# Kernel tuning notes

Measured on AMD Instinct MI355X. Metric: run time of the kernel, lower is better.

The kernel has to match this reference:

```python
import jax, jax.numpy as jnp
import numpy as np

EPS = 1e-5  # torch BatchNorm2d default eps

def _bn(x, gamma, beta):
    # training-mode batch statistics over (N,H,W), per channel (biased variance)
    mean = jnp.mean(x, axis=(0, 2, 3), keepdims=True)
    var = jnp.var(x, axis=(0, 2, 3), keepdims=True)
    return gamma[None, :, None, None] * (x - mean) * jax.lax.rsqrt(var + EPS) + beta[None, :, None, None]

def _conv1x1(x, w, b):
    # (B,C,H,W) x (O,C) -> (B,O,H,W)
    return jnp.einsum('bchw,oc->bohw', x, w) + b[None, :, None, None]

def _maxpool2(x):
    B, C, H, W = x.shape
    return x.reshape(B, C, H // 2, 2, W // 2, 2).max(axis=(3, 5))

def setup_inputs() -> dict:
    key = jax.random.key(0)
    ks = jax.random.split(key, 5)
    B, C, H, W = 16, 256, 56, 56
    Ci, Cg = C // 8, C // 4
    def kaiming(k, o, i):
        return jax.random.normal(k, (o, i), jnp.float32) * np.float32(np.sqrt(2.0 / i))
    return {
        'x': jax.random.normal(ks[0], (B, C, H, W), jnp.float32),
        'bn1_gamma': jnp.ones((C,), jnp.float32),
        'bn1_beta': jnp.zeros((C,), jnp.float32),
        'w_g': kaiming(ks[1], Cg, C), 'b_g': jnp.zeros((Cg,), jnp.float32),
        'w_theta': kaiming(ks[2], Ci, C), 'b_theta': jnp.zeros((Ci,), jnp.float32),
        'w_phi': kaiming(ks[3], Ci, C), 'b_phi': jnp.zeros((Ci,), jnp.float32),
        'bn2_gamma': jnp.ones((Cg,), jnp.float32),
        'bn2_beta': jnp.zeros((Cg,), jnp.float32),
        'w_z': kaiming(ks[4], C, Cg), 'b_z': jnp.zeros((C,), jnp.float32),
    }

def reference(x, bn1_gamma, bn1_beta, w_g, b_g, w_theta, b_theta, w_phi, b_phi, bn2_gamma, bn2_beta, w_z, b_z):
    identity = x
    B, C, H, W = x.shape
    xa = jax.nn.relu(_bn(x, bn1_gamma, bn1_beta))
    g_x = _maxpool2(_conv1x1(xa, w_g, b_g))        # (B,Cg,H/2,W/2)
    phi_x = _maxpool2(_conv1x1(xa, w_phi, b_phi))  # (B,Ci,H/2,W/2)
    theta_x = _conv1x1(xa, w_theta, b_theta)       # (B,Ci,H,W)
    Cg = g_x.shape[1]
    Ci = theta_x.shape[1]
    Np = g_x.shape[2] * g_x.shape[3]               # subsampled positions (H/2*W/2)
    g_x = g_x.reshape(B, Cg, Np).transpose(0, 2, 1)      # (B,Np,Cg)
    phi_x = phi_x.reshape(B, Ci, Np)                     # (B,Ci,Np)
    theta_x = theta_x.reshape(B, Ci, H * W).transpose(0, 2, 1)  # (B,HW,Ci)
    f_div_C = jnp.einsum('bnc,bcm->bnm', theta_x, phi_x) / Np   # (B,HW,Np)
    y = jnp.einsum('bnm,bmc->bnc', f_div_C, g_x)                # (B,HW,Cg)
    y = y.transpose(0, 2, 1).reshape(B, Cg, H, W)
    w_y = _conv1x1(jax.nn.relu(_bn(y, bn2_gamma, bn2_beta)), w_z, b_z)
    return w_y + identity
```

## Files before the change

### kernel.cpp

```cpp
#include <hip/hip_runtime.h>
#include <hip/hip_bf16.h>

#define BB 16
#define CC 256
#define HWN 3136
#define NCI 32
#define NPP 784

typedef __attribute__((ext_vector_type(8))) short short8;
typedef __attribute__((ext_vector_type(4))) float floatx4;

__device__ __forceinline__ unsigned short f2bf(float f) {
    union { __hip_bfloat16 h; unsigned short u; } cv;
    cv.h = __float2bfloat16(f);
    return cv.u;
}
__device__ __forceinline__ float bf2f(unsigned short u) {
    return __uint_as_float(((unsigned)u) << 16);
}

__device__ __forceinline__ void stage_Tt(unsigned short* Tt, const unsigned short* th,
                                         int b, int hw0, int tid) {
    int p2 = tid & 15, hwq = tid >> 4;
    int c0 = 2 * p2;
    const unsigned short* tb = th + (size_t)(b * NCI) * HWN + hw0 + hwq * 4;
    ushort4 v0 = *(const ushort4*)(tb + (size_t)c0 * HWN);
    ushort4 v1 = *(const ushort4*)(tb + (size_t)(c0 + 1) * HWN);
    unsigned int* tw = (unsigned int*)Tt;
    tw[(hwq * 4 + 0) * 20 + p2] = (unsigned)v0.x | ((unsigned)v1.x << 16);
    tw[(hwq * 4 + 1) * 20 + p2] = (unsigned)v0.y | ((unsigned)v1.y << 16);
    tw[(hwq * 4 + 2) * 20 + p2] = (unsigned)v0.z | ((unsigned)v1.z << 16);
    tw[(hwq * 4 + 3) * 20 + p2] = (unsigned)v0.w | ((unsigned)v1.w << 16);
}

__global__ __launch_bounds__(256) void k_head(const float* __restrict__ x,
                                              const float* __restrict__ w_t,
                                              const float* __restrict__ w_p,
                                              const float* __restrict__ w_g,
                                              const float* __restrict__ w_z,
                                              unsigned short* __restrict__ wcat,
                                              unsigned short* __restrict__ wzb,
                                              unsigned short* __restrict__ pool,
                                              float* __restrict__ zacc,
                                              float* __restrict__ bn1part) {
    int blk = blockIdx.x;
    int c = threadIdx.x;
    if (blk < 128) {
        int o = blk;
        const float* src = (o < 32) ? (w_t + o * CC)
                          : (o < 64) ? (w_p + (o - 32) * CC)
                                     : (w_g + (o - 64) * CC);
        wcat[o * CC + c] = f2bf(src[c]);
        {
            int r = o * 2 + (c >> 7);
            int kk = c & 127;
            if (kk < 72)
                wzb[r * 72 + kk] = (kk < 64) ? f2bf(w_z[r * 64 + kk]) : (unsigned short)0;
        }
        if (o < 96) {
            int b = c >> 4, kk = c & 15;
            pool[((size_t)(b * 96 + o)) * 800 + 784 + kk] = 0;
        }
        int idx = o * 256 + c;
        if (idx < 17024) zacc[idx] = 0.f;
        return;
    }
    int bc = blk - 128;
    const float4* p = (const float4*)(x + (size_t)bc * HWN);
    int tid = c;
    float s = 0.f, q = 0.f;
    for (int i = tid; i < 784; i += 256) {
        float4 v = p[i];
        s += v.x + v.y + v.z + v.w;
        q += v.x * v.x + v.y * v.y + v.z * v.z + v.w * v.w;
    }
    #pragma unroll
    for (int off = 32; off > 0; off >>= 1) {
        s += __shfl_down(s, off);
        q += __shfl_down(q, off);
    }
    __shared__ float sh[16];
    int wid = tid >> 6, lane = tid & 63;
    if (lane == 0) { sh[wid] = s; sh[8 + wid] = q; }
    __syncthreads();
    if (tid == 0) bn1part[bc]        = sh[0] + sh[1] + sh[2] + sh[3];
    if (tid == 1) bn1part[4096 + bc] = sh[8] + sh[9] + sh[10] + sh[11];
}

__global__ __launch_bounds__(512) void k_conv1(const float* __restrict__ x,
                                               const unsigned short* __restrict__ wcat,
                                               const float* __restrict__ bn1part,
                                               const float* __restrict__ gamma,
                                               const float* __restrict__ beta,
                                               const float* __restrict__ b_g,
                                               const float* __restrict__ b_t,
                                               const float* __restrict__ b_p,
                                               unsigned short* __restrict__ th,
                                               unsigned short* __restrict__ pool,
                                               float* __restrict__ T1g,
                                               float* __restrict__ Gg) {
    int b  = blockIdx.y;
    int bx = blockIdx.x;
    int hw0 = bx * 112;
    int tid = threadIdx.x;
    int wv = tid >> 6, ln = tid & 63;
    int col = ln & 15, quad = ln >> 4;

    __shared__ unsigned short smem[128 * 120];
    unsigned short* As = smem;
    unsigned short* Bs = smem + 4096;
    __shared__ float ab_s[512];
    __shared__ float bias_s[128];

    if (tid < 256) {
        const float inv = 1.0f / (BB * HWN);
        float s = 0.f, q = 0.f;
        #pragma unroll
        for (int b2 = 0; b2 < BB; ++b2) {
            s += bn1part[b2 * 256 + tid];
            q += bn1part[4096 + b2 * 256 + tid];
        }
        float mean = s * inv;
        float var  = q * inv - mean * mean;
        float a = gamma[tid] * rsqrtf(var + 1e-5f);
        ab_s[tid] = a;
        ab_s[CC + tid] = beta[tid] - mean * a;
    }
    if (tid < 128) {
        int o = tid;
        bias_s[o] = (o < 32) ? b_t[o] : (o < 64) ? b_p[o - 32] : b_g[o - 64];
    }
    __syncthreads();

    floatx4 acc[7];
    #pragma unroll
    for (int nt = 0; nt < 7; ++nt)
        acc[nt] = (floatx4){0.f, 0.f, 0.f, 0.f};

    int p   = tid & 15;
    int hwq = tid >> 4;
    bool act = hwq < 28;
    const float* xb = x + (size_t)(b * CC) * HWN + hw0;

    float4 pv0, pv1;
    if (act) {
        int c0 = 2 * p;
        pv0 = *(const float4*)(xb + (size_t)c0 * HWN + hwq * 4);
        pv1 = *(const float4*)(xb + (size_t)(c0 + 1) * HWN + hwq * 4);
    }

    for (int k0 = 0; k0 < CC; k0 += 32) {
        {
            const unsigned short* gp = wcat + (wv * 16 + (ln >> 2)) * CC + k0 + (ln & 3) * 8;
            __builtin_amdgcn_global_load_lds(
                (const __attribute__((address_space(1))) unsigned int*)gp,
                (__attribute__((address_space(3))) unsigned int*)&As[wv * 512],
                16, 0, 0);
        }
        if (act) {
            int c0 = k0 + 2 * p;
            float a0 = ab_s[c0],     d0 = ab_s[CC + c0];
            float a1 = ab_s[c0 + 1], d1 = ab_s[CC + c0 + 1];
            unsigned int* bw = (unsigned int*)Bs;
            float r0[4] = { fmaxf(fmaf(a0, pv0.x, d0), 0.f), fmaxf(fmaf(a0, pv0.y, d0), 0.f),
                            fmaxf(fmaf(a0, pv0.z, d0), 0.f), fmaxf(fmaf(a0, pv0.w, d0), 0.f) };
            float r1[4] = { fmaxf(fmaf(a1, pv1.x, d1), 0.f), fmaxf(fmaf(a1, pv1.y, d1), 0.f),
                            fmaxf(fmaf(a1, pv1.z, d1), 0.f), fmaxf(fmaf(a1, pv1.w, d1), 0.f) };
            #pragma unroll
            for (int i = 0; i < 4; ++i) {
                unsigned int w = (unsigned int)f2bf(r0[i]) | ((unsigned int)f2bf(r1[i]) << 16);
                bw[(hwq * 4 + i) * 16 + p] = w;
            }
        }
        __syncthreads();

        if (act && k0 + 32 < CC) {
            int c0 = k0 + 32 + 2 * p;
            pv0 = *(const float4*)(xb + (size_t)c0 * HWN + hwq * 4);
            pv1 = *(const float4*)(xb + (size_t)(c0 + 1) * HWN + hwq * 4);
        }

        short8 af = *(const short8*)&As[(wv * 16 + col) * 32 + quad * 8];
        #pragma unroll
        for (int nt = 0; nt < 7; ++nt) {
            short8 bf = *(const short8*)&Bs[(nt * 16 + col) * 32 + quad * 8];
            acc[nt] = __builtin_amdgcn_mfma_f32_16x16x32_bf16(af, bf, acc[nt], 0, 0, 0);
        }
        __syncthreads();
    }

    unsigned short* Ct = smem;
    {
        int obase = wv * 16 + quad * 4;
        #pragma unroll
        for (int r = 0; r < 4; ++r) {
            float bias = bias_s[obase + r];
            #pragma unroll
            for (int nt = 0; nt < 7; ++nt)
                Ct[(obase + r) * 120 + nt * 16 + col] = f2bf(acc[nt][r] + bias);
        }
    }
    __syncthreads();

    #pragma unroll
    for (int i = 0; i < 2; ++i) {
        int e = tid + i * 512;
        if (e < 896) {
            int ch = e / 28, c4 = e - ch * 28;
            ushort4 v = *(const ushort4*)&Ct[ch * 120 + c4 * 4];
            *(ushort4*)&th[((size_t)(b * NCI + ch)) * HWN + hw0 + c4 * 4] = v;
        }
    }
    {
        int row = tid >> 4;
        int seg = tid & 15;
        float s = 0.f;
        #pragma unroll
        for (int j = 0; j < 7; ++j) s += bf2f(Ct[row * 120 + seg * 7 + j]);
        s += __shfl_down(s, 8);
        s += __shfl_down(s, 4);
        s += __shfl_down(s, 2);
        s += __shfl_down(s, 1);
        if (seg == 0) atomicAdd(&T1g[b * NCI + row], s);
    }
    {
        int m = (wv >> 1) & 1, n = wv & 1;
        int ks0 = (wv >> 2) * 2;
        floatx4 g = (floatx4){0.f, 0.f, 0.f, 0.f};
        short8 z8 = (short8){0, 0, 0, 0, 0, 0, 0, 0};
        #pragma unroll
        for (int kx = 0; kx < 2; ++kx) {
            int ks = ks0 + kx;
            short8 ga, gb;
            if (ks < 3 || quad < 2) {
                ga = *(const short8*)&Ct[(m * 16 + col) * 120 + ks * 32 + quad * 8];
                gb = *(const short8*)&Ct[(n * 16 + col) * 120 + ks * 32 + quad * 8];
            } else {
                ga = z8; gb = z8;
            }
            g = __builtin_amdgcn_mfma_f32_16x16x32_bf16(ga, gb, g, 0, 0, 0);
        }
        float* ggp = Gg + b * 1024 + (m * 16 + quad * 4) * 32 + n * 16 + col;
        #pragma unroll
        for (int r = 0; r < 4; ++r) atomicAdd(&ggp[r * 32], g[r]);
    }
    #pragma unroll
    for (int i = 0; i < 6; ++i) {
        int e = tid + i * 512;
        if (e < 2688) {
            int ch = e / 28, m = e - ch * 28;
            const unsigned short* r0p = &Ct[(32 + ch) * 120 + 2 * m];
            float v = fmaxf(fmaxf(bf2f(r0p[0]), bf2f(r0p[1])),
                            fmaxf(bf2f(r0p[56]), bf2f(r0p[57])));
            pool[((size_t)(b * 96 + ch)) * 800 + bx * 28 + m] = f2bf(v);
        }
    }
}

__global__ __launch_bounds__(256) void k_sgemm(const unsigned short* __restrict__ pool,
                                               const float* __restrict__ T1g,
                                               const float* __restrict__ Gg,
                                               unsigned short* __restrict__ Sg,
                                               float* __restrict__ bn2acc) {
    int q = blockIdx.x;
    int b = blockIdx.y;
    int tid = threadIdx.x;
    int wv = tid >> 6, ln = tid & 63;
    int col = ln & 15, quad = ln >> 4;
    __shared__ float Sred[4 * 512];
    __shared__ float Gred[1024];
    __shared__ float T1s[32];
    __shared__ float shs[16], shq[16];

    if (tid < 16) { shs[tid] = 0.f; shq[tid] = 0.f; }
    if (tid < 32) T1s[tid] = T1g[b * NCI + tid];
    for (int idx = tid; idx < 1024; idx += 256) Gred[idx] = Gg[b * 1024 + idx];

    const unsigned short* gbase = pool + ((size_t)(b * 96 + 32 + q * 16)) * 800;
    const unsigned short* pbase = pool + ((size_t)(b * 96)) * 800;
    floatx4 acc[2];
    acc[0] = (floatx4){0.f, 0.f, 0.f, 0.f};
    acc[1] = (floatx4){0.f, 0.f, 0.f, 0.f};
    for (int ks = wv; ks < 25; ks += 4) {
        int k0 = ks * 32;
        short8 af = *(const short8*)&gbase[(size_t)col * 800 + k0 + quad * 8];
        #pragma unroll
        for (int nt = 0; nt < 2; ++nt) {
            short8 bf = *(const short8*)&pbase[(nt * 16 + col) * 800 + k0 + quad * 8];
            acc[nt] = __builtin_amdgcn_mfma_f32_16x16x32_bf16(af, bf, acc[nt], 0, 0, 0);
        }
    }
    #pragma unroll
    for (int nt = 0; nt < 2; ++nt)
        for (int r = 0; r < 4; ++r)
            Sred[wv * 512 + (quad * 4 + r) * 32 + nt * 16 + col] = acc[nt][r];
    __syncthreads();

    for (int idx = tid; idx < 512; idx += 256) {
        float s = Sred[idx] + Sred[512 + idx] + Sred[1024 + idx] + Sred[1536 + idx];
        int cgl = idx >> 5, ci = idx & 31;
        unsigned short h = f2bf(s * (1.0f / NPP));
        Sg[(size_t)b * 2560 + (q * 16 + cgl) * 40 + ci] = h;
        Sred[idx] = bf2f(h);
    }
    __syncthreads();

    {
        int cgl = tid & 15, part = tid >> 4;
        float sum = 0.f, sq = 0.f;
        #pragma unroll
        for (int i = 0; i < 2; ++i) {
            int ci = part * 2 + i;
            float sv = Sred[cgl * 32 + ci];
            sum += sv * T1s[ci];
            float t2 = 0.f;
            #pragma unroll
            for (int cj = 0; cj < 32; ++cj)
                t2 += Gred[ci * 32 + cj] * Sred[cgl * 32 + cj];
            sq += sv * t2;
        }
        atomicAdd(&shs[cgl], sum);
        atomicAdd(&shq[cgl], sq);
    }
    __syncthreads();
    if (tid < 16) {
        atomicAdd(&bn2acc[q * 16 + tid], shs[tid]);
        atomicAdd(&bn2acc[64 + q * 16 + tid], shq[tid]);
    }
}

__global__ __launch_bounds__(256) void k_convz(const unsigned short* __restrict__ th,
                                               const unsigned short* __restrict__ Sg,
                                               const unsigned short* __restrict__ wzb,
                                               const float* __restrict__ bn2acc,
                                               const float* __restrict__ gamma,
                                               const float* __restrict__ beta,
                                               const float* __restrict__ b_z,
                                               const float* __restrict__ x,
                                               float* __restrict__ out) {
    int b = blockIdx.y;
    int hw0 = blockIdx.x * 64;
    int tid = threadIdx.x;
    int wv = tid >> 6, ln = tid & 63;
    int col = ln & 15, quad = ln >> 4;

    __shared__ unsigned short Wl[256 * 72];
    __shared__ unsigned short TS[5120];
    __shared__ float ab2_s[128];
    unsigned short* Tt = TS;
    unsigned short* St = TS + 2560;
    unsigned short* Yt = TS;

    for (int j = wv; j < 36; j += 4) {
        const unsigned short* gp = wzb + j * 512 + ln * 8;
        __builtin_amdgcn_global_load_lds(
            (const __attribute__((address_space(1))) unsigned int*)gp,
            (__attribute__((address_space(3))) unsigned int*)&Wl[j * 512],
            16, 0, 0);
    }
    if (tid < 64) {
        const float inv = 1.0f / (BB * HWN);
        float mean = bn2acc[tid] * inv;
        float var  = bn2acc[64 + tid] * inv - mean * mean;
        float a = gamma[tid] * rsqrtf(var + 1e-5f);
        ab2_s[tid] = a;
        ab2_s[64 + tid] = beta[tid] - mean * a;
    }
    {
        const unsigned int* sgw = (const unsigned int*)(Sg + (size_t)b * 2560);
        unsigned int* stw = (unsigned int*)St;
        for (int i = tid; i < 1280; i += 256) stw[i] = sgw[i];
    }
    stage_Tt(Tt, th, b, hw0, tid);
    __syncthreads();

    short8 afy = *(const short8*)&Tt[(wv * 16 + col) * 40 + quad * 8];
    floatx4 yacc[4];
    #pragma unroll
    for (int nt = 0; nt < 4; ++nt) {
        short8 bf = *(const short8*)&St[(nt * 16 + col) * 40 + quad * 8];
        floatx4 z = (floatx4){0.f, 0.f, 0.f, 0.f};
        yacc[nt] = __builtin_amdgcn_mfma_f32_16x16x32_bf16(afy, bf, z, 0, 0, 0);
    }
    __syncthreads();

    #pragma unroll
    for (int nt = 0; nt < 4; ++nt) {
        int cg = nt * 16 + col;
        float a = ab2_s[cg], d = ab2_s[64 + cg];
        #pragma unroll
        for (int r = 0; r < 4; ++r) {
            int hwl = wv * 16 + quad * 4 + r;
            Yt[hwl * 72 + cg] = f2bf(fmaxf(fmaf(a, yacc[nt][r], d), 0.f));
        }
    }
    __syncthreads();

    floatx4 acc[16];
    #pragma unroll
    for (int nt = 0; nt < 16; ++nt) acc[nt] = (floatx4){0.f, 0.f, 0.f, 0.f};

    #pragma unroll
    for (int kk = 0; kk < 2; ++kk) {
        short8 afm = *(const short8*)&Yt[(wv * 16 + col) * 72 + kk * 32 + quad * 8];
        #pragma unroll
        for (int nt = 0; nt < 16; ++nt) {
            short8 bf = *(const short8*)&Wl[(nt * 16 + col) * 72 + kk * 32 + quad * 8];
            acc[nt] = __builtin_amdgcn_mfma_f32_16x16x32_bf16(afm, bf, acc[nt], 0, 0, 0);
        }
    }

    #pragma unroll
    for (int nt = 0; nt < 16; ++nt) {
        int co = nt * 16 + col;
        size_t base = ((size_t)(b * CC + co)) * HWN + hw0 + wv * 16 + quad * 4;
        float4 xv = *(const float4*)&x[base];
        float bz = b_z[co];
        float4 r = make_float4(acc[nt][0] + bz + xv.x, acc[nt][1] + bz + xv.y,
                               acc[nt][2] + bz + xv.z, acc[nt][3] + bz + xv.w);
        *(float4*)&out[base] = r;
    }
}

extern "C" void kernel_launch(void* const* d_in, const int* in_sizes, int n_in,
                              void* d_out, int out_size, void* d_ws, size_t ws_size,
                              hipStream_t stream) {
    (void)in_sizes; (void)n_in; (void)out_size; (void)ws_size;
    const float* x   = (const float*)d_in[0];
    const float* g1  = (const float*)d_in[1];
    const float* b1  = (const float*)d_in[2];
    const float* w_g = (const float*)d_in[3];
    const float* b_g = (const float*)d_in[4];
    const float* w_t = (const float*)d_in[5];
    const float* b_t = (const float*)d_in[6];
    const float* w_p = (const float*)d_in[7];
    const float* b_p = (const float*)d_in[8];
    const float* g2  = (const float*)d_in[9];
    const float* b2  = (const float*)d_in[10];
    const float* w_z = (const float*)d_in[11];
    const float* b_z = (const float*)d_in[12];
    float* out = (float*)d_out;

    float* ws      = (float*)d_ws;
    float* bn1part = ws;
    float* zacc    = ws + 8192;
    float* bn2acc  = ws + 8192;
    float* T1g     = ws + 8320;
    float* Gg      = ws + 8832;
    unsigned short* wcat = (unsigned short*)(ws + 25216);
    unsigned short* wzb  = (unsigned short*)(ws + 41600);
    unsigned short* th   = (unsigned short*)(ws + 50816);
    unsigned short* pool = (unsigned short*)(ws + 853632);
    unsigned short* Sg   = (unsigned short*)(ws + 1468032);

    k_head  <<<dim3(4224),     dim3(256), 0, stream>>>(x, w_t, w_p, w_g, w_z, wcat, wzb, pool, zacc, bn1part);
    k_conv1 <<<dim3(28, BB),   dim3(512), 0, stream>>>(x, wcat, bn1part, g1, b1, b_g, b_t, b_p, th, pool, T1g, Gg);
    k_sgemm <<<dim3(4, BB),    dim3(256), 0, stream>>>(pool, T1g, Gg, Sg, bn2acc);
    k_convz <<<dim3(49, BB),   dim3(256), 0, stream>>>(th, Sg, wzb, bn2acc, g2, b2, b_z, x, out);
}
```

Before: 170.1 us.

## Double-buffer LDS tiles in projection GEMM with one barrier per k-step

The projection GEMM k-loop now ping-pongs between two LDS buffers for the weight (A) and activation (B) tiles. The next weight tile is prefetched asynchronously via global_load_lds right after the barrier, and explicit s_waitcnt counts replace __syncthreads, removing the second barrier per iteration. Inactive threads clamp their load address so the vmcnt accounting stays uniform. This relies on hand-tuned waitcnt values and uses more LDS, which risks correctness if the counts do not match the outstanding loads.

```diff
diff --git a/kernel.cpp b/kernel.cpp
--- a/kernel.cpp
+++ b/kernel.cpp
@@ -107,8 +107,6 @@
     int col = ln & 15, quad = ln >> 4;
 
     __shared__ unsigned short smem[128 * 120];
-    unsigned short* As = smem;
-    unsigned short* Bs = smem + 4096;
     __shared__ float ab_s[512];
     __shared__ float bias_s[128];
 
@@ -137,26 +135,34 @@
     for (int nt = 0; nt < 7; ++nt)
         acc[nt] = (floatx4){0.f, 0.f, 0.f, 0.f};
 
-    int p   = tid & 15;
-    int hwq = tid >> 4;
+    int p    = tid & 15;
+    int hwq  = tid >> 4;
     bool act = hwq < 28;
+    int hwqc = act ? hwq : 27;
     const float* xb = x + (size_t)(b * CC) * HWN + hw0;
 
+    {
+        const unsigned short* gp = wcat + (wv * 16 + (ln >> 2)) * CC + (ln & 3) * 8;
+        __builtin_amdgcn_global_load_lds(
+            (const __attribute__((address_space(1))) unsigned int*)gp,
+            (__attribute__((address_space(3))) unsigned int*)&smem[wv * 512],
+            16, 0, 0);
+    }
+    __builtin_amdgcn_sched_barrier(0);
     float4 pv0, pv1;
-    if (act) {
+    {
         int c0 = 2 * p;
-        pv0 = *(const float4*)(xb + (size_t)c0 * HWN + hwq * 4);
-        pv1 = *(const float4*)(xb + (size_t)(c0 + 1) * HWN + hwq * 4);
-    }
-
-    for (int k0 = 0; k0 < CC; k0 += 32) {
-        {
-            const unsigned short* gp = wcat + (wv * 16 + (ln >> 2)) * CC + k0 + (ln & 3) * 8;
-            __builtin_amdgcn_global_load_lds(
-                (const __attribute__((address_space(1))) unsigned int*)gp,
-                (__attribute__((address_space(3))) unsigned int*)&As[wv * 512],
-                16, 0, 0);
-        }
+        pv0 = *(const float4*)(xb + (size_t)c0 * HWN + hwqc * 4);
+        pv1 = *(const float4*)(xb + (size_t)(c0 + 1) * HWN + hwqc * 4);
+    }
+
+    #pragma unroll
+    for (int k = 0; k < 8; ++k) {
+        int k0 = k * 32;
+        int cur = k & 1;
+        unsigned short* As = smem + cur * 4096;
+        unsigned short* Bs = smem + 8192 + cur * 3584;
+
         if (act) {
             int c0 = k0 + 2 * p;
             float a0 = ab_s[c0],     d0 = ab_s[CC + c0];
@@ -172,12 +178,26 @@
                 bw[(hwq * 4 + i) * 16 + p] = w;
             }
         }
-        __syncthreads();
-
-        if (act && k0 + 32 < CC) {
+        if (k < 7) {
             int c0 = k0 + 32 + 2 * p;
-            pv0 = *(const float4*)(xb + (size_t)c0 * HWN + hwq * 4);
-            pv1 = *(const float4*)(xb + (size_t)(c0 + 1) * HWN + hwq * 4);
+            pv0 = *(const float4*)(xb + (size_t)c0 * HWN + hwqc * 4);
+            pv1 = *(const float4*)(xb + (size_t)(c0 + 1) * HWN + hwqc * 4);
+        }
+        if (k < 7)
+            asm volatile("s_waitcnt vmcnt(2) lgkmcnt(0)" ::: "memory");
+        else
+            asm volatile("s_waitcnt vmcnt(0) lgkmcnt(0)" ::: "memory");
+        __builtin_amdgcn_s_barrier();
+        __builtin_amdgcn_sched_barrier(0);
+
+        if (k < 7) {
+            unsigned short* Asn = smem + (cur ^ 1) * 4096;
+            const unsigned short* gp = wcat + (wv * 16 + (ln >> 2)) * CC + (k0 + 32) + (ln & 3) * 8;
+            __builtin_amdgcn_global_load_lds(
+                (const __attribute__((address_space(1))) unsigned int*)gp,
+                (__attribute__((address_space(3))) unsigned int*)&Asn[wv * 512],
+                16, 0, 0);
+            __builtin_amdgcn_sched_barrier(0);
         }
 
         short8 af = *(const short8*)&As[(wv * 16 + col) * 32 + quad * 8];
@@ -186,8 +206,8 @@
             short8 bf = *(const short8*)&Bs[(nt * 16 + col) * 32 + quad * 8];
             acc[nt] = __builtin_amdgcn_mfma_f32_16x16x32_bf16(af, bf, acc[nt], 0, 0, 0);
         }
-        __syncthreads();
-    }
+    }
+    __syncthreads();
 
     unsigned short* Ct = smem;
     {
```

Measured after the change: 172.2 us. About the same (+1.2%).
